# Kernel tuning notes

Hardware: AMD Instinct MI355X
Metric: run time of the kernel (lower is better)

## Reference

```python
import jax, jax.numpy as jnp
import numpy as np

# Constants from the SaffronNet repo (assumed values)
NUM_VARIABLES = 3
MAX_POS_DIST = 20.0    # MAX_ANOT_ANCHOR_POSITION_DISTANCE
MAX_ANG_DIST = 15.0    # MAX_ANOT_ANCHOR_ANGLE_DISTANCE
ALPHA = 0.95
GAMMA = 2.0
EPS = 1e-4

B, A, C, M = 8, 131072, 4, 64
IMG = 512.0


def setup_inputs() -> dict:
    key = jax.random.key(0)
    k1, k2, k3, k4, k5, k6 = jax.random.split(key, 6)
    classifications = jax.random.uniform(k1, (B, A, C), dtype=jnp.float32,
                                         minval=0.001, maxval=0.999)
    regressions = jax.random.normal(k2, (B, A, 3), dtype=jnp.float32) * 5.0
    # anchors: (1, A, 3) -> (x, y, alpha)
    xy = jax.random.uniform(k3, (1, A, 2), dtype=jnp.float32) * IMG
    al = jax.random.uniform(k4, (1, A, 1), dtype=jnp.float32) * 90.0
    anchors = jnp.concatenate([xy, al], axis=-1)
    # annotations: (B, M, 4) -> (x, y, alpha, label); last 16 rows padded with label=-1
    axy = jax.random.uniform(k5, (B, M, 2), dtype=jnp.float32) * IMG
    aal = jax.random.uniform(k6, (B, M, 1), dtype=jnp.float32) * 90.0
    lab = jax.random.randint(jax.random.fold_in(key, 7), (B, M, 1), 0, C).astype(jnp.float32)
    lab = lab.at[:, M - 16:, :].set(-1.0)  # padding (invalid annotations)
    annotations = jnp.concatenate([axy, aal, lab], axis=-1)
    return {"classifications": classifications, "regressions": regressions,
            "anchors": anchors, "annotations": annotations}


def _per_sample(classification, regression, annot, anchor):
    valid = annot[:, NUM_VARIABLES] != -1.0                      # (M,)
    cls = jnp.clip(classification, EPS, 1.0 - EPS)
    # pairwise |anchor - annot| distances, invalid annotations masked to +inf
    dx = jnp.abs(anchor[:, 0, None] - annot[None, :, 0])          # (A, M)
    dy = jnp.abs(anchor[:, 1, None] - annot[None, :, 1])
    dalpha = jnp.abs(anchor[:, 2, None] - annot[None, :, 2])
    dxy = jnp.sqrt(dx * dx + dy * dy)
    dxy = jnp.where(valid[None, :], dxy, jnp.inf)
    dxy_min = jnp.min(dxy, axis=1)                                # (A,)
    dxy_argmin = jnp.argmin(dxy, axis=1)                          # (A,)
    a = jnp.take_along_axis(dalpha, dxy_argmin[:, None], axis=1)[:, 0]
    positive = (dxy_min < MAX_POS_DIST) & (a < MAX_ANG_DIST)      # (A,)
    # targets: start at -1 (ignore); far anchors -> 0; positives -> one-hot
    background = (dxy_min >= 1.5 * MAX_POS_DIST) | (a >= 1.5 * MAX_ANG_DIST)
    t = jnp.full((classification.shape[0], classification.shape[1]), -1.0)
    t = jnp.where(background[:, None], 0.0, t)
    t = jnp.where(positive[:, None], 0.0, t)
    assigned = annot[dxy_argmin]                                  # (A, 4)
    label = jnp.clip(assigned[:, NUM_VARIABLES].astype(jnp.int32), 0, classification.shape[1] - 1)
    onehot = jax.nn.one_hot(label, classification.shape[1], dtype=jnp.float32)
    t = jnp.where(positive[:, None] & (onehot > 0.5), 1.0, t)
    num_pos = jnp.sum(positive.astype(jnp.float32))
    denom = jnp.maximum(num_pos, 1.0)
    # focal loss (ignore t == -1 entries)
    alpha_factor = jnp.where(t == 1.0, ALPHA, 1.0 - ALPHA)
    focal_weight = alpha_factor * jnp.where(t == 1.0, 1.0 - cls, cls) ** GAMMA
    bce = -(t * jnp.log(cls) + (1.0 - t) * jnp.log(1.0 - cls))
    cls_loss = jnp.where(t != -1.0, focal_weight * bce, 0.0)
    cls_total = jnp.sum(cls_loss) / denom
    tgt = assigned[:, :NUM_VARIABLES] - anchor                    # (A, 3): dx, dy, dalpha
    posf = positive.astype(jnp.float32)
    diff_xy = jnp.abs(tgt[:, :2] - regression[:, :2])             # (A, 2)
    loss_xy = jnp.where(diff_xy <= 1.0 / 9.0, 0.5 * 9.0 * diff_xy ** 2, diff_xy - 0.5 / 9.0)
    xy_total = jnp.sum(loss_xy * posf[:, None]) / (2.0 * denom)   # mean over pos rows x 2 cols
    diff_ang = jnp.maximum((jnp.abs(tgt[:, 2] - regression[:, 2]) - 10.0) / 5.0, 0.0)
    ang_total = jnp.sum(diff_ang * posf) / denom
    return cls_total, xy_total, ang_total


def reference(classifications, regressions, anchors, annotations):
    anchor = anchors[0]  # (A, 3)
    cls_l, xy_l, ang_l = jax.vmap(_per_sample, in_axes=(0, 0, 0, None))(
        classifications, regressions, annotations, anchor)
    return jnp.stack([jnp.mean(cls_l), jnp.mean(xy_l), jnp.mean(ang_l)])
```

## Files before the change

kernel.cpp:

```cpp
#include <hip/hip_runtime.h>
#include <cmath>

#define NUM_B 8
#define NUM_C 4
#define NUM_M 64
#define APT   8
#define BLK   256
constexpr float MAX_POS_D2  = 20.0f * 20.0f;
constexpr float BG_POS_D2   = 30.0f * 30.0f;
constexpr float MAX_ANG     = 15.0f;
constexpr float BG_ANG      = 22.5f;
constexpr float ALPHA_C     = 0.95f;
constexpr float EPS_C       = 1e-4f;

__global__ __launch_bounds__(BLK) void focal_main(
    const float* __restrict__ cls,
    const float* __restrict__ reg,
    const float* __restrict__ anc,
    const float* __restrict__ ann,
    double* __restrict__ ws,
    int A)
{
    const int b    = blockIdx.y;
    const int tid  = threadIdx.x;
    const int base = blockIdx.x * (BLK * APT);

    float ax[APT], ay[APT], aal[APT];
    float4 cv[APT];
    float rx[APT], ry[APT], ra[APT];
    #pragma unroll
    for (int j = 0; j < APT; ++j) {
        const int a  = base + tid + j * BLK;
        const int ac = min(a, A - 1);
        const float* ap = anc + 3 * (size_t)ac;
        ax[j] = ap[0]; ay[j] = ap[1]; aal[j] = ap[2];
        cv[j] = *(const float4*)(cls + ((size_t)b * A + ac) * NUM_C);
        const float* rp = reg + ((size_t)b * A + ac) * 3;
        rx[j] = rp[0]; ry[j] = rp[1]; ra[j] = rp[2];
    }

    __shared__ float4 s_mins[NUM_M];
    __shared__ float4 s_ann[NUM_M];
    if (tid < NUM_M) {
        const float4 an = ((const float4*)(ann + (size_t)b * NUM_M * 4))[tid];
        const bool valid = (an.w != -1.0f);
        const float rh = valid ? 0.5f * fmaf(an.x, an.x, an.y * an.y) : 1e36f;
        s_mins[tid] = make_float4(an.x, an.y, rh, 0.0f);
        s_ann[tid]  = an;
    }
    __syncthreads();

    float ub[APT];
    int   ubi[APT];
    #pragma unroll
    for (int j = 0; j < APT; ++j) { ub[j] = -INFINITY; ubi[j] = 0; }

    #pragma unroll 16
    for (int m = 0; m < NUM_M; ++m) {
        const float4 an = s_mins[m];
        #pragma unroll
        for (int j = 0; j < APT; ++j) {
            const float t = fmaf(ay[j], an.y, -an.z);
            const float u = fmaf(ax[j], an.x, t);
            const bool gt = u > ub[j];
            ub[j]  = gt ? u : ub[j];
            ubi[j] = gt ? m : ubi[j];
        }
    }

    float cls_s = 0.0f, xy_s = 0.0f, ang_s = 0.0f, pos_s = 0.0f;

    #pragma unroll
    for (int j = 0; j < APT; ++j) {
        const int a = base + tid + j * BLK;
        if (a >= A) continue;

        const float q  = fmaf(ax[j], ax[j], ay[j] * ay[j]);
        const float d2 = fmaf(-2.0f, ub[j], q);
        const float4 ba = s_ann[ubi[j]];
        const float  dal = fabsf(aal[j] - ba.z);

        const bool positive   = (d2 < MAX_POS_D2) && (dal < MAX_ANG);
        const bool background = (d2 >= BG_POS_D2) || (dal >= BG_ANG);

        int label = (int)ba.w;
        label = min(max(label, 0), NUM_C - 1);

        const float cc[4] = {cv[j].x, cv[j].y, cv[j].z, cv[j].w};
        float acc = 0.0f;
        #pragma unroll
        for (int c = 0; c < NUM_C; ++c) {
            const float p = fminf(fmaxf(cc[c], EPS_C), 1.0f - EPS_C);
            const bool is1  = positive && (c == label);
            const float r   = is1 ? (1.0f - p) : p;
            const float af  = is1 ? ALPHA_C : (1.0f - ALPHA_C);
            const float omr = is1 ? p : (1.0f - p);
            acc += af * r * r * (-__logf(omr));
        }
        cls_s += (positive || background) ? acc : 0.0f;

        if (positive) {
            pos_s += 1.0f;
            const float dxr = fabsf((ba.x - ax[j]) - rx[j]);
            const float dyr = fabsf((ba.y - ay[j]) - ry[j]);
            const float lx = (dxr <= 1.0f / 9.0f) ? 4.5f * dxr * dxr : dxr - 1.0f / 18.0f;
            const float ly = (dyr <= 1.0f / 9.0f) ? 4.5f * dyr * dyr : dyr - 1.0f / 18.0f;
            xy_s += lx + ly;
            const float dar = fabsf((ba.z - aal[j]) - ra[j]);
            ang_s += fmaxf((dar - 10.0f) * 0.2f, 0.0f);
        }
    }

    #pragma unroll
    for (int off = 32; off > 0; off >>= 1) {
        cls_s += __shfl_down(cls_s, off, 64);
        xy_s  += __shfl_down(xy_s,  off, 64);
        ang_s += __shfl_down(ang_s, off, 64);
        pos_s += __shfl_down(pos_s, off, 64);
    }
    __shared__ float s_red[BLK / 64][4];
    const int wave = tid >> 6;
    const int lane = tid & 63;
    if (lane == 0) {
        s_red[wave][0] = cls_s;
        s_red[wave][1] = xy_s;
        s_red[wave][2] = ang_s;
        s_red[wave][3] = pos_s;
    }
    __syncthreads();
    if (tid == 0) {
        float c0 = 0.0f, c1 = 0.0f, c2 = 0.0f, c3 = 0.0f;
        #pragma unroll
        for (int w = 0; w < BLK / 64; ++w) {
            c0 += s_red[w][0];
            c1 += s_red[w][1];
            c2 += s_red[w][2];
            c3 += s_red[w][3];
        }
        atomicAdd(&ws[b * 4 + 0], (double)c0);
        atomicAdd(&ws[b * 4 + 1], (double)c1);
        atomicAdd(&ws[b * 4 + 2], (double)c2);
        atomicAdd(&ws[b * 4 + 3], (double)c3);
    }
}

__global__ void focal_finalize(const double* __restrict__ ws, float* __restrict__ out)
{
    if (threadIdx.x == 0) {
        double sc = 0.0, sx = 0.0, sg = 0.0;
        #pragma unroll
        for (int b = 0; b < NUM_B; ++b) {
            const double denom = fmax(ws[b * 4 + 3], 1.0);
            sc += ws[b * 4 + 0] / denom;
            sx += ws[b * 4 + 1] / (2.0 * denom);
            sg += ws[b * 4 + 2] / denom;
        }
        out[0] = (float)(sc / (double)NUM_B);
        out[1] = (float)(sx / (double)NUM_B);
        out[2] = (float)(sg / (double)NUM_B);
    }
}

extern "C" void kernel_launch(void* const* d_in, const int* in_sizes, int n_in,
                              void* d_out, int out_size, void* d_ws, size_t ws_size,
                              hipStream_t stream)
{
    const float* cls = (const float*)d_in[0];
    const float* reg = (const float*)d_in[1];
    const float* anc = (const float*)d_in[2];
    const float* ann = (const float*)d_in[3];
    const int A = in_sizes[2] / 3;

    double* ws = (double*)d_ws;
    hipMemsetAsync(d_ws, 0, NUM_B * 4 * sizeof(double), stream);

    dim3 grid((A + BLK * APT - 1) / (BLK * APT), NUM_B);
    focal_main<<<grid, BLK, 0, stream>>>(cls, reg, anc, ann, ws, A);
    focal_finalize<<<1, 64, 0, stream>>>(ws, (float*)d_out);
}
```

Measured before the change: 100.5 us.

## Fuse finalize into main kernel via last-block counter and halve anchors per thread

```diff
diff --git a/kernel.cpp b/kernel.cpp
--- a/kernel.cpp
+++ b/kernel.cpp
@@ -4,7 +4,7 @@
 #define NUM_B 8
 #define NUM_C 4
 #define NUM_M 64
-#define APT   8
+#define APT   4
 #define BLK   256
 constexpr float MAX_POS_D2  = 20.0f * 20.0f;
 constexpr float BG_POS_D2   = 30.0f * 30.0f;
@@ -19,11 +19,16 @@
     const float* __restrict__ anc,
     const float* __restrict__ ann,
     double* __restrict__ ws,
-    int A)
+    float* __restrict__ out,
+    int A, int total_blocks)
 {
     const int b    = blockIdx.y;
     const int tid  = threadIdx.x;
     const int base = blockIdx.x * (BLK * APT);
+
+    float4 an_raw;
+    if (tid < NUM_M)
+        an_raw = ((const float4*)(ann + (size_t)b * NUM_M * 4))[tid];
 
     float ax[APT], ay[APT], aal[APT];
     float4 cv[APT];
@@ -42,7 +47,7 @@
     __shared__ float4 s_mins[NUM_M];
     __shared__ float4 s_ann[NUM_M];
     if (tid < NUM_M) {
-        const float4 an = ((const float4*)(ann + (size_t)b * NUM_M * 4))[tid];
+        const float4 an = an_raw;
         const bool valid = (an.w != -1.0f);
         const float rh = valid ? 0.5f * fmaf(an.x, an.x, an.y * an.y) : 1e36f;
         s_mins[tid] = make_float4(an.x, an.y, rh, 0.0f);
@@ -128,6 +133,7 @@
         s_red[wave][3] = pos_s;
     }
     __syncthreads();
+
     if (tid == 0) {
         float c0 = 0.0f, c1 = 0.0f, c2 = 0.0f, c3 = 0.0f;
         #pragma unroll
@@ -141,23 +147,28 @@
         atomicAdd(&ws[b * 4 + 1], (double)c1);
         atomicAdd(&ws[b * 4 + 2], (double)c2);
         atomicAdd(&ws[b * 4 + 3], (double)c3);
-    }
-}
 
-__global__ void focal_finalize(const double* __restrict__ ws, float* __restrict__ out)
-{
-    if (threadIdx.x == 0) {
-        double sc = 0.0, sx = 0.0, sg = 0.0;
-        #pragma unroll
-        for (int b = 0; b < NUM_B; ++b) {
-            const double denom = fmax(ws[b * 4 + 3], 1.0);
-            sc += ws[b * 4 + 0] / denom;
-            sx += ws[b * 4 + 1] / (2.0 * denom);
-            sg += ws[b * 4 + 2] / denom;
+        __threadfence();
+        int* counter = (int*)(ws + NUM_B * 4);
+        const int old = atomicAdd(counter, 1);
+        if (old == total_blocks - 1) {
+            __threadfence();
+            double sc = 0.0, sx = 0.0, sg = 0.0;
+            #pragma unroll
+            for (int bb = 0; bb < NUM_B; ++bb) {
+                const double s0 = __hip_atomic_load(&ws[bb * 4 + 0], __ATOMIC_RELAXED, __HIP_MEMORY_SCOPE_AGENT);
+                const double s1 = __hip_atomic_load(&ws[bb * 4 + 1], __ATOMIC_RELAXED, __HIP_MEMORY_SCOPE_AGENT);
+                const double s2 = __hip_atomic_load(&ws[bb * 4 + 2], __ATOMIC_RELAXED, __HIP_MEMORY_SCOPE_AGENT);
+                const double s3 = __hip_atomic_load(&ws[bb * 4 + 3], __ATOMIC_RELAXED, __HIP_MEMORY_SCOPE_AGENT);
+                const double denom = fmax(s3, 1.0);
+                sc += s0 / denom;
+                sx += s1 / (2.0 * denom);
+                sg += s2 / denom;
+            }
+            out[0] = (float)(sc / (double)NUM_B);
+            out[1] = (float)(sx / (double)NUM_B);
+            out[2] = (float)(sg / (double)NUM_B);
         }
-        out[0] = (float)(sc / (double)NUM_B);
-        out[1] = (float)(sx / (double)NUM_B);
-        out[2] = (float)(sg / (double)NUM_B);
     }
 }
 
@@ -172,9 +183,10 @@
     const int A = in_sizes[2] / 3;
 
     double* ws = (double*)d_ws;
-    hipMemsetAsync(d_ws, 0, NUM_B * 4 * sizeof(double), stream);
+    hipMemsetAsync(d_ws, 0, (NUM_B * 4 + 1) * sizeof(double), stream);
 
     dim3 grid((A + BLK * APT - 1) / (BLK * APT), NUM_B);
-    focal_main<<<grid, BLK, 0, stream>>>(cls, reg, anc, ann, ws, A);
-    focal_finalize<<<1, 64, 0, stream>>>(ws, (float*)d_out);
+    const int total_blocks = grid.x * grid.y;
+    focal_main<<<grid, BLK, 0, stream>>>(cls, reg, anc, ann, ws, (float*)d_out,
+                                         A, total_blocks);
 }
```

New measurement: 120.5 us. +19.9%, slower.
